# Performance work log

Hardware: AMD Instinct MI355X
Metric: run time of the kernel (lower is better)

Reference implementation:

```python
import jax, jax.numpy as jnp
import numpy as np

L, H, Wn, C = 2048, 768, 1024, 64


def setup_inputs() -> dict:
    key = jax.random.key(0)
    ks = jax.random.split(key, 12)
    s = 1.0 / np.sqrt(H)
    s3 = 1.0 / np.sqrt(3 * H)
    return {
        "tok_embs": jax.random.normal(ks[0], (L, H), jnp.float32),
        "wmask": jax.random.randint(ks[1], (L,), 0, Wn + 1),  # 1-indexed word positions, 0 = ignore
        "text_length": Wn,
        "label_embs": jax.random.normal(ks[2], (C, H), jnp.float32),
        "W_tok": jax.random.normal(ks[3], (H, 2 * H), jnp.float32) * s,
        "b_tok": jnp.zeros((2 * H,), jnp.float32),
        "W_lab": jax.random.normal(ks[4], (H, 2 * H), jnp.float32) * s,
        "b_lab": jnp.zeros((2 * H,), jnp.float32),
        "W1": jax.random.normal(ks[5], (3 * H, H), jnp.float32) * s3,
        "b1": jnp.zeros((H,), jnp.float32),
        "W2": jax.random.normal(ks[6], (H, 3), jnp.float32) * s,
        "b2": jnp.zeros((3,), jnp.float32),
    }


def reference(tok_embs, wmask, text_length, label_embs, W_tok, b_tok, W_lab, b_lab, W1, b1, W2, b2):
    Wd = text_length
    Hd = tok_embs.shape[-1]
    # --- word-level scatter pooling: we[wmask-1] = tok_embs where wmask > 0 ---
    # route masked-out tokens to a dummy row Wd, then drop it (jit-safe, no nonzero)
    tgt = jnp.where(wmask > 0, wmask - 1, Wd)
    we = jnp.zeros((Wd + 1, Hd), tok_embs.dtype).at[tgt].set(tok_embs)[:Wd]  # (W, H)
    # --- scorer ---
    t = (we @ W_tok + b_tok).reshape(Wd, 2, Hd)        # (W, 2, H)
    lb = (label_embs @ W_lab + b_lab).reshape(-1, 2, Hd)  # (C, 2, H)
    Cd = lb.shape[0]
    t0 = jnp.broadcast_to(t[:, None, 0, :], (Wd, Cd, Hd))
    l0 = jnp.broadcast_to(lb[None, :, 0, :], (Wd, Cd, Hd))
    prod = t[:, None, 1, :] * lb[None, :, 1, :]        # (W, C, H)
    cat = jnp.concatenate([t0, l0, prod], axis=-1)     # (W, C, 3H)
    h = jax.nn.relu(cat @ W1 + b1)                     # (W, C, H)
    scores = h @ W2 + b2                               # (W, C, 3)
    return scores
```

## Files before the change

### kernel.cpp

```cpp
#include <hip/hip_runtime.h>
#include <hip/hip_bf16.h>

static constexpr int Hd = 768;
static constexpr int H2 = 1536;
static constexpr int Cn = 64;

typedef __attribute__((ext_vector_type(8))) short short8;
typedef __attribute__((ext_vector_type(8))) _Float16 half8;
typedef __attribute__((ext_vector_type(4))) float f32x4;
typedef unsigned short us;

__device__ inline unsigned int f2bf2(float a, float b) {
    __hip_bfloat162 h = __float22bfloat162_rn(float2{a, b});
    return *reinterpret_cast<unsigned int*>(&h);
}

__device__ inline void split1(float x, us& h, us& l) {
    __hip_bfloat16 hb = __float2bfloat16(x);
    float hf = __bfloat162float(hb);
    __hip_bfloat16 lb_ = __float2bfloat16(x - hf);
    h = *reinterpret_cast<us*>(&hb);
    l = *reinterpret_cast<us*>(&lb_);
}

__device__ inline us f2b(float x) {
    __hip_bfloat16 b = __float2bfloat16(x);
    return *reinterpret_cast<us*>(&b);
}

__device__ inline us f2h(float x) {
    _Float16 h = (_Float16)x;
    return *reinterpret_cast<us*>(&h);
}

__device__ inline float b2f(us u) {
    __hip_bfloat16 b = *reinterpret_cast<__hip_bfloat16*>(&u);
    return __bfloat162float(b);
}

__device__ inline short8 hmul8(short8 a, short8 b) {
    half8 x = __builtin_bit_cast(half8, a);
    half8 y = __builtin_bit_cast(half8, b);
    half8 r = x * y;
    return __builtin_bit_cast(short8, r);
}

__device__ inline void gload16(const void* g, void* l) {
    __builtin_amdgcn_global_load_lds(
        (const __attribute__((address_space(1))) unsigned int*)g,
        (__attribute__((address_space(3))) unsigned int*)l, 16, 0, 0);
}

__global__ void k_init(int* widx, int Wd) {
    int i = blockIdx.x * 256 + threadIdx.x;
    if (i < Wd) widx[i] = -1;
}

__global__ void k_scatter(const int* __restrict__ wmask, int* widx, int L, int Wd) {
    int i = blockIdx.x * 256 + threadIdx.x;
    if (i < L) {
        int m = wmask[i];
        if (m > 0 && m <= Wd) atomicMax(&widx[m - 1], i);
    }
}

__global__ void k_build_we_split(const float4* __restrict__ tok, const int* __restrict__ widx,
                                 us* __restrict__ weh, us* __restrict__ wel, int Wd) {
    int i = blockIdx.x * 256 + threadIdx.x;
    if (i >= Wd * 192) return;
    int w = i / 192, c4 = i - w * 192;
    int idx = widx[w];
    float4 v = (idx >= 0) ? tok[idx * 192 + c4] : float4{0.f, 0.f, 0.f, 0.f};
    us hh[4], ll[4];
    split1(v.x, hh[0], ll[0]);
    split1(v.y, hh[1], ll[1]);
    split1(v.z, hh[2], ll[2]);
    split1(v.w, hh[3], ll[3]);
    size_t o = (size_t)w * Hd + c4 * 4;
    *(ushort4*)&weh[o] = ushort4{hh[0], hh[1], hh[2], hh[3]};
    *(ushort4*)&wel[o] = ushort4{ll[0], ll[1], ll[2], ll[3]};
}

struct TSArgs {
    const float* src[5];
    us* th[5];
    us* tl[5];
    int ld[5];
    int N[5];
    int fmt[5];
};
__global__ __launch_bounds__(256)
void k_tsplit(TSArgs a) {
    __shared__ float tile[64][65];
    const int z = blockIdx.z;
    const int n0 = blockIdx.x * 64, k0 = blockIdx.y * 64;
    if (n0 >= a.N[z]) return;
    const float* W = a.src[z];
    const int ld = a.ld[z];
    for (int idx = threadIdx.x; idx < 4096; idx += 256) {
        int kk = idx >> 6, nn = idx & 63;
        tile[kk][nn] = W[(size_t)(k0 + kk) * ld + n0 + nn];
    }
    __syncthreads();
    us* Th = a.th[z];
    us* Tl = a.tl[z];
    const int fmt = a.fmt[z];
    for (int idx = threadIdx.x; idx < 4096; idx += 256) {
        int nn = idx >> 6, kk = idx & 63;
        size_t o = (size_t)(n0 + nn) * Hd + k0 + kk;
        if (fmt) {
            Th[o] = f2h(tile[kk][nn]);
        } else {
            us h, l;
            split1(tile[kk][nn], h, l);
            Th[o] = h;
            Tl[o] = l;
        }
    }
}

__global__ __launch_bounds__(256)
void k_split(const float* __restrict__ x, int lda, int cols,
             us* __restrict__ h, us* __restrict__ l, int n4) {
    int i = blockIdx.x * 256 + threadIdx.x;
    if (i >= n4) return;
    int c4 = cols >> 2;
    int row = i / c4, cc = (i - row * c4) * 4;
    float4 v = *(const float4*)&x[(size_t)row * lda + cc];
    us hh[4], ll[4];
    split1(v.x, hh[0], ll[0]);
    split1(v.y, hh[1], ll[1]);
    split1(v.z, hh[2], ll[2]);
    split1(v.w, hh[3], ll[3]);
    size_t o = (size_t)row * cols + cc;
    *(ushort4*)&h[o] = ushort4{hh[0], hh[1], hh[2], hh[3]};
    *(ushort4*)&l[o] = ushort4{ll[0], ll[1], ll[2], ll[3]};
}

__global__ __launch_bounds__(256)
void k_gemm2(const us* __restrict__ Ah, const us* __restrict__ Al,
             const us* __restrict__ BhT, const us* __restrict__ BlT,
             float* __restrict__ Cpart, int M, int N, int K) {
    __shared__ __align__(16) us S[2][4][64 * 32];
    const int tid = threadIdx.x, wave = tid >> 6, lane = tid & 63;
    const int quad = lane >> 4, l15 = lane & 15;
    const int wm = wave & 1, wn = wave >> 1;
    const int m0 = blockIdx.y * 64, n0 = blockIdx.x * 64;
    const int Ks = K / gridDim.z, kbeg = blockIdx.z * Ks, kend = kbeg + Ks;
    float* C = Cpart + (size_t)blockIdx.z * M * N;

    const int srow = wave * 16 + (lane >> 2), soff = (lane & 3) * 8;
    const size_t gaB = (size_t)(m0 + srow) * K + soff;
    const size_t gbB = (size_t)(n0 + srow) * K + soff;
    const int lo = wave * 16 * 32;

    f32x4 acc[2][2];
#pragma unroll
    for (int a = 0; a < 2; ++a)
#pragma unroll
        for (int b = 0; b < 2; ++b) acc[a][b] = (f32x4){0.f, 0.f, 0.f, 0.f};

    auto stage = [&](int p, int k0) {
        gload16(Ah + gaB + k0, &S[p][0][lo]);
        gload16(Al + gaB + k0, &S[p][1][lo]);
        gload16(BhT + gbB + k0, &S[p][2][lo]);
        gload16(BlT + gbB + k0, &S[p][3][lo]);
    };

    int p = 0;
    stage(0, kbeg);
    for (int k0 = kbeg; k0 < kend; k0 += 32) {
        __syncthreads();
        if (k0 + 32 < kend) stage(p ^ 1, k0 + 32);
        short8 ah[2], al[2], bh[2], bl[2];
#pragma unroll
        for (int mt = 0; mt < 2; ++mt) {
            int off = (wm * 32 + mt * 16 + l15) * 32 + quad * 8;
            ah[mt] = *(const short8*)&S[p][0][off];
            al[mt] = *(const short8*)&S[p][1][off];
        }
#pragma unroll
        for (int nt = 0; nt < 2; ++nt) {
            int off = (wn * 32 + nt * 16 + l15) * 32 + quad * 8;
            bh[nt] = *(const short8*)&S[p][2][off];
            bl[nt] = *(const short8*)&S[p][3][off];
        }
#pragma unroll
        for (int mt = 0; mt < 2; ++mt)
#pragma unroll
            for (int nt = 0; nt < 2; ++nt) {
                acc[mt][nt] = __builtin_amdgcn_mfma_f32_16x16x32_bf16(al[mt], bh[nt], acc[mt][nt], 0, 0, 0);
                acc[mt][nt] = __builtin_amdgcn_mfma_f32_16x16x32_bf16(ah[mt], bl[nt], acc[mt][nt], 0, 0, 0);
                acc[mt][nt] = __builtin_amdgcn_mfma_f32_16x16x32_bf16(ah[mt], bh[nt], acc[mt][nt], 0, 0, 0);
            }
        p ^= 1;
    }
#pragma unroll
    for (int mt = 0; mt < 2; ++mt)
#pragma unroll
        for (int nt = 0; nt < 2; ++nt) {
            int col = n0 + wn * 32 + nt * 16 + l15;
#pragma unroll
            for (int reg = 0; reg < 4; ++reg) {
                int row = m0 + wm * 32 + mt * 16 + quad * 4 + reg;
                C[(size_t)row * N + col] = acc[mt][nt][reg];
            }
        }
}

__global__ __launch_bounds__(256)
void k_gemm3(const us* __restrict__ Ah, const us* __restrict__ Al,
             const us* __restrict__ BhT, const us* __restrict__ BlT,
             const float* __restrict__ bias, float* __restrict__ outF,
             us* __restrict__ sh, us* __restrict__ sl, us* __restrict__ bh16,
             int fp16out, int scols, int N, int K) {
    __shared__ __align__(16) us S[2][4][64 * 32];
    const int tid = threadIdx.x, wave = tid >> 6, lane = tid & 63;
    const int quad = lane >> 4, l15 = lane & 15;
    const int wm = wave & 1, wn = wave >> 1;
    const int m0 = blockIdx.y * 64, n0 = blockIdx.x * 64;

    const int srow = wave * 16 + (lane >> 2), soff = (lane & 3) * 8;
    const size_t gaB = (size_t)(m0 + srow) * K + soff;
    const size_t gbB = (size_t)(n0 + srow) * K + soff;
    const int lo = wave * 16 * 32;

    f32x4 acc[2][2];
#pragma unroll
    for (int a = 0; a < 2; ++a)
#pragma unroll
        for (int b = 0; b < 2; ++b) acc[a][b] = (f32x4){0.f, 0.f, 0.f, 0.f};

    auto stage = [&](int p, int k0) {
        gload16(Ah + gaB + k0, &S[p][0][lo]);
        gload16(Al + gaB + k0, &S[p][1][lo]);
        gload16(BhT + gbB + k0, &S[p][2][lo]);
        gload16(BlT + gbB + k0, &S[p][3][lo]);
    };

    int p = 0;
    stage(0, 0);
    for (int k0 = 0; k0 < K; k0 += 32) {
        __syncthreads();
        if (k0 + 32 < K) stage(p ^ 1, k0 + 32);
        short8 ah[2], al[2], bh[2], bl[2];
#pragma unroll
        for (int mt = 0; mt < 2; ++mt) {
            int off = (wm * 32 + mt * 16 + l15) * 32 + quad * 8;
            ah[mt] = *(const short8*)&S[p][0][off];
            al[mt] = *(const short8*)&S[p][1][off];
        }
#pragma unroll
        for (int nt = 0; nt < 2; ++nt) {
            int off = (wn * 32 + nt * 16 + l15) * 32 + quad * 8;
            bh[nt] = *(const short8*)&S[p][2][off];
            bl[nt] = *(const short8*)&S[p][3][off];
        }
#pragma unroll
        for (int mt = 0; mt < 2; ++mt)
#pragma unroll
            for (int nt = 0; nt < 2; ++nt) {
                acc[mt][nt] = __builtin_amdgcn_mfma_f32_16x16x32_bf16(al[mt], bh[nt], acc[mt][nt], 0, 0, 0);
                acc[mt][nt] = __builtin_amdgcn_mfma_f32_16x16x32_bf16(ah[mt], bl[nt], acc[mt][nt], 0, 0, 0);
                acc[mt][nt] = __builtin_amdgcn_mfma_f32_16x16x32_bf16(ah[mt], bh[nt], acc[mt][nt], 0, 0, 0);
            }
        p ^= 1;
    }
#pragma unroll
    for (int mt = 0; mt < 2; ++mt)
#pragma unroll
        for (int nt = 0; nt < 2; ++nt) {
            int col = n0 + wn * 32 + nt * 16 + l15;
            float bb = bias ? bias[col] : 0.f;
#pragma unroll
            for (int reg = 0; reg < 4; ++reg) {
                int row = m0 + wm * 32 + mt * 16 + quad * 4 + reg;
                float v = acc[mt][nt][reg] + bb;
                if (outF) outF[(size_t)row * N + col] = v;
                if (sh) {
                    if (col < scols) {
                        us h, l;
                        split1(v, h, l);
                        size_t o = (size_t)row * scols + col;
                        sh[o] = h;
                        sl[o] = l;
                    } else if (bh16) {
                        bh16[(size_t)row * scols + (col - scols)] = fp16out ? f2h(v) : f2b(v);
                    }
                }
            }
        }
}

__global__ __launch_bounds__(256)
void k_reduce(const float* __restrict__ part, int S, int MN, int N,
              const float* __restrict__ bias, float* __restrict__ outF,
              us* __restrict__ sh, us* __restrict__ sl, int scols,
              us* __restrict__ bh16, int fp16out) {
    int i = blockIdx.x * 256 + threadIdx.x;
    if (i >= MN) return;
    float v = 0.f;
    for (int s = 0; s < S; ++s) v += part[(size_t)s * MN + i];
    int row = i / N, col = i - row * N;
    if (bias) v += bias[col];
    if (outF) outF[i] = v;
    if (col < scols) {
        if (sh) {
            us h, l;
            split1(v, h, l);
            size_t o = (size_t)row * scols + col;
            sh[o] = h;
            sl[o] = l;
        }
    } else if (bh16) {
        bh16[(size_t)row * scols + (col - scols)] = fp16out ? f2h(v) : f2b(v);
    }
}

__global__ __launch_bounds__(256, 2)
void k_mfma10(const us* __restrict__ t1b,
              const us* __restrict__ W1ct,
              const us* __restrict__ lb1b,
              const float* __restrict__ Aw,
              const float* __restrict__ Bc,
              const float* __restrict__ W2,
              float* __restrict__ scr) {
    __shared__ __align__(16) us As[3][4096];
    __shared__ __align__(16) us Bs[3][4096];
    __shared__ __align__(16) us lbs[2][Hd];
    __shared__ float sred[2 * 128 * 3];

    const int tid = threadIdx.x, wave = tid >> 6, lane = tid & 63;
    const int quad = lane >> 4, l15 = lane & 15;
    const int wm = wave & 1, wn = wave >> 1;

    const int b = blockIdx.x;
    const int xcd = b & 7, slot = b >> 3;
    const int jx = slot >> 5;
    const int cp = slot & 31;
    const int c0 = cp * 2;
    const int jt = jx * 128, m0 = xcd * 128;

    for (int i = tid; i < 2 * 128 * 3; i += 256) sred[i] = 0.f;
    if (tid < 192) {
        int cc = tid / 96, o = (tid - cc * 96) * 8;
        *(short8*)&lbs[cc][o] = *(const short8*)&lb1b[(size_t)(c0 + cc) * Hd + o];
    }

    const int srow = (wave & 1) * 64 + lane;
    const int skq = (wave >> 1) * 8;
    const us* gA = W1ct + (size_t)(jt + srow) * Hd + skq;
    const us* gB = t1b + (size_t)(m0 + srow) * Hd + skq;

    f32x4 acc0[4][4], acc1[4][4];
#pragma unroll
    for (int mt = 0; mt < 4; ++mt)
#pragma unroll
        for (int nt = 0; nt < 4; ++nt) {
            acc0[mt][nt] = (f32x4){0.f, 0.f, 0.f, 0.f};
            acc1[mt][nt] = (f32x4){0.f, 0.f, 0.f, 0.f};
        }

    auto stageT = [&](int p, int k0) {
        gload16(gA + k0,      &As[p][wave * 512]);
        gload16(gA + k0 + 16, &As[p][(wave + 4) * 512]);
        gload16(gB + k0,      &Bs[p][wave * 512]);
        gload16(gB + k0 + 16, &Bs[p][(wave + 4) * 512]);
    };

    const int rbA = quad * 1024 + (wm * 64 + l15) * 8;
    const int rbB = quad * 1024 + (wn * 64 + l15) * 8;

    auto readFrags = [&](short8 (&af)[4], short8 (&bf)[4], short8& l0, short8& l1,
                         int buf, int k0) {
        const us* Ab = &As[buf][0];
        const us* Bb = &Bs[buf][0];
#pragma unroll
        for (int mt = 0; mt < 4; ++mt) af[mt] = *(const short8*)&Ab[rbA + mt * 128];
#pragma unroll
        for (int nt = 0; nt < 4; ++nt) bf[nt] = *(const short8*)&Bb[rbB + nt * 128];
        l0 = *(const short8*)&lbs[0][k0 + quad * 8];
        l1 = *(const short8*)&lbs[1][k0 + quad * 8];
    };

    auto cluster = [&](const short8 (&af)[4], const short8 (&bf)[4],
                       const short8& l0, const short8& l1) {
        __builtin_amdgcn_s_setprio(1);
#pragma unroll
        for (int mt = 0; mt < 4; ++mt) {
            short8 a0 = hmul8(af[mt], l0);
            short8 a1 = hmul8(af[mt], l1);
#pragma unroll
            for (int nt = 0; nt < 4; ++nt) {
                acc0[mt][nt] = __builtin_amdgcn_mfma_f32_16x16x32_f16(
                    __builtin_bit_cast(half8, a0),
                    __builtin_bit_cast(half8, bf[nt]), acc0[mt][nt], 0, 0, 0);
                acc1[mt][nt] = __builtin_amdgcn_mfma_f32_16x16x32_f16(
                    __builtin_bit_cast(half8, a1),
                    __builtin_bit_cast(half8, bf[nt]), acc1[mt][nt], 0, 0, 0);
            }
        }
        __builtin_amdgcn_s_setprio(0);
    };

    __syncthreads();

    stageT(0, 0);
    stageT(1, 32);
    asm volatile("s_waitcnt vmcnt(4)" ::: "memory");
    __builtin_amdgcn_s_barrier();
    __builtin_amdgcn_sched_barrier(0);

    short8 afA[4], bfA[4], lvA0, lvA1;
    short8 afB[4], bfB[4], lvB0, lvB1;
    readFrags(afA, bfA, lvA0, lvA1, 0, 0);

    int bc = 0, bn = 1, bs = 2;
    for (int i = 0; i < 24; i += 2) {
        if (i + 1 < 24) {
            asm volatile("s_waitcnt vmcnt(0)" ::: "memory");
            __builtin_amdgcn_s_barrier();
            __builtin_amdgcn_sched_barrier(0);
            readFrags(afB, bfB, lvB0, lvB1, bn, (i + 1) * 32);
            if (i + 2 < 24) stageT(bs, (i + 2) * 32);
            int t = bc; bc = bn; bn = bs; bs = t;
            __builtin_amdgcn_sched_barrier(0);
        }
        cluster(afA, bfA, lvA0, lvA1);
        if (i + 2 < 24) {
            asm volatile("s_waitcnt vmcnt(0)" ::: "memory");
            __builtin_amdgcn_s_barrier();
            __builtin_amdgcn_sched_barrier(0);
            readFrags(afA, bfA, lvA0, lvA1, bn, (i + 2) * 32);
            if (i + 3 < 24) stageT(bs, (i + 3) * 32);
            int t = bc; bc = bn; bn = bs; bs = t;
            __builtin_amdgcn_sched_barrier(0);
        }
        cluster(afB, bfB, lvB0, lvB1);
    }

    float bcv0[4][4], bcv1[4][4], w2v[4][4][3];
#pragma unroll
    for (int mt = 0; mt < 4; ++mt) {
        const int jb = jt + wm * 64 + mt * 16 + quad * 4;
        float4 b4 = *(const float4*)&Bc[(size_t)c0 * Hd + jb];
        bcv0[mt][0] = b4.x; bcv0[mt][1] = b4.y; bcv0[mt][2] = b4.z; bcv0[mt][3] = b4.w;
        float4 b5 = *(const float4*)&Bc[(size_t)(c0 + 1) * Hd + jb];
        bcv1[mt][0] = b5.x; bcv1[mt][1] = b5.y; bcv1[mt][2] = b5.z; bcv1[mt][3] = b5.w;
#pragma unroll
        for (int reg = 0; reg < 4; ++reg)
#pragma unroll
            for (int r = 0; r < 3; ++r) w2v[mt][reg][r] = W2[(jb + reg) * 3 + r];
    }

    auto reduce_c = [&](const f32x4 (&ac)[4][4], const float (&bcv)[4][4], int cc) {
#pragma unroll
        for (int nt = 0; nt < 4; ++nt) {
            const int w = m0 + wn * 64 + nt * 16 + l15;
            const float* awp = Aw + (size_t)w * Hd + jt + wm * 64;
            float s0 = 0.f, s1 = 0.f, s2 = 0.f;
#pragma unroll
            for (int mt = 0; mt < 4; ++mt) {
                float4 a4 = *(const float4*)&awp[mt * 16 + quad * 4];
                float av[4] = {a4.x, a4.y, a4.z, a4.w};
#pragma unroll
                for (int reg = 0; reg < 4; ++reg) {
                    float h = ac[mt][nt][reg] + av[reg] + bcv[mt][reg];
                    h = h > 0.f ? h : 0.f;
                    s0 += h * w2v[mt][reg][0];
                    s1 += h * w2v[mt][reg][1];
                    s2 += h * w2v[mt][reg][2];
                }
            }
            s0 += __shfl_xor(s0, 16); s0 += __shfl_xor(s0, 32);
            s1 += __shfl_xor(s1, 16); s1 += __shfl_xor(s1, 32);
            s2 += __shfl_xor(s2, 16); s2 += __shfl_xor(s2, 32);
            if (quad == 0) {
                const int wl = wn * 64 + nt * 16 + l15;
                atomicAdd(&sred[cc * 384 + wl * 3 + 0], s0);
                atomicAdd(&sred[cc * 384 + wl * 3 + 1], s1);
                atomicAdd(&sred[cc * 384 + wl * 3 + 2], s2);
            }
        }
    };
    reduce_c(acc0, bcv0, 0);
    reduce_c(acc1, bcv1, 1);
    __syncthreads();

    float* slab = scr + ((size_t)jx * 1024 * Cn + (size_t)m0 * Cn) * 3;
    for (int i = tid; i < 2 * 128 * 3; i += 256) {
        int cc = i / 384, j = i - cc * 384;
        int wl = j / 3, r = j - wl * 3;
        slab[((size_t)wl * Cn + (c0 + cc)) * 3 + r] = sred[i];
    }
}

__global__ __launch_bounds__(256)
void k_scores(const float* __restrict__ scr, const float* __restrict__ b2,
              float* __restrict__ out, int n) {
    int i = blockIdx.x * 256 + threadIdx.x;
    if (i >= n) return;
    float v = b2[i % 3];
#pragma unroll
    for (int s = 0; s < 6; ++s) v += scr[(size_t)s * n + i];
    out[i] = v;
}

extern "C" void kernel_launch(void* const* d_in, const int* in_sizes, int n_in,
                              void* d_out, int out_size, void* d_ws, size_t ws_size,
                              hipStream_t stream) {
    const float* tok    = (const float*)d_in[0];
    const int*   wmask  = (const int*)d_in[1];
    const float* labe   = (const float*)d_in[3];
    const float* W_tok  = (const float*)d_in[4];
    const float* b_tok  = (const float*)d_in[5];
    const float* W_lab  = (const float*)d_in[6];
    const float* b_lab  = (const float*)d_in[7];
    const float* W1     = (const float*)d_in[8];
    const float* b1     = (const float*)d_in[9];
    const float* W2     = (const float*)d_in[10];
    const float* b2     = (const float*)d_in[11];
    float* out = (float*)d_out;

    const int L  = in_sizes[1];
    const int Wd = out_size / (Cn * 3);

    char* ws = (char*)d_ws;
    size_t off = 0;
    auto alloc = [&](size_t bytes) { char* p = ws + off; off += (bytes + 255) & ~(size_t)255; return p; };
    int*   widx  = (int*)alloc(4096);
    float* Abuf  = (float*)alloc((size_t)Wd * Hd * 4);
    float* Bbuf  = (float*)alloc((size_t)Cn * Hd * 4);
    us* W1ct  = (us*)alloc((size_t)Hd * Hd * 2);
    us* W1cl  = (us*)alloc((size_t)Hd * Hd * 2);
    us* t1b   = (us*)alloc((size_t)Wd * Hd * 2);
    us* lb1b  = (us*)alloc((size_t)Cn * Hd * 2);
    float* scr = (float*)alloc((size_t)6 * Wd * Cn * 3 * 4);
    us* WtTh  = (us*)alloc((size_t)H2 * Hd * 2);
    us* WtTl  = (us*)alloc((size_t)H2 * Hd * 2);
    us* WlTh  = (us*)alloc((size_t)H2 * Hd * 2);
    us* WlTl  = (us*)alloc((size_t)H2 * Hd * 2);
    us* W1aTh = (us*)alloc((size_t)Hd * Hd * 2);
    us* W1aTl = (us*)alloc((size_t)Hd * Hd * 2);
    us* W1bTh = (us*)alloc((size_t)Hd * Hd * 2);
    us* W1bTl = (us*)alloc((size_t)Hd * Hd * 2);
    us* weh   = (us*)alloc((size_t)Wd * Hd * 2);
    us* wel   = (us*)alloc((size_t)Wd * Hd * 2);
    us* lah   = (us*)alloc((size_t)Cn * Hd * 2);
    us* lal   = (us*)alloc((size_t)Cn * Hd * 2);
    us* t0h   = (us*)alloc((size_t)Wd * Hd * 2);
    us* t0l   = (us*)alloc((size_t)Wd * Hd * 2);
    us* lb0h  = (us*)alloc((size_t)Cn * Hd * 2);
    us* lb0l  = (us*)alloc((size_t)Cn * Hd * 2);
    float* part = (float*)alloc((size_t)8 * Cn * H2 * 4);

    k_init<<<(Wd + 255) / 256, 256, 0, stream>>>(widx, Wd);
    k_scatter<<<(L + 255) / 256, 256, 0, stream>>>(wmask, widx, L, Wd);
    k_build_we_split<<<(Wd * 192 + 255) / 256, 256, 0, stream>>>((const float4*)tok, widx, weh, wel, Wd);

    TSArgs ts;
    ts.src[0] = W_tok;  ts.th[0] = WtTh;  ts.tl[0] = WtTl;  ts.ld[0] = H2; ts.N[0] = H2; ts.fmt[0] = 0;
    ts.src[1] = W_lab;  ts.th[1] = WlTh;  ts.tl[1] = WlTl;  ts.ld[1] = H2; ts.N[1] = H2; ts.fmt[1] = 0;
    ts.src[2] = W1;                         ts.th[2] = W1aTh; ts.tl[2] = W1aTl; ts.ld[2] = Hd; ts.N[2] = Hd; ts.fmt[2] = 0;
    ts.src[3] = W1 + (size_t)Hd * Hd;       ts.th[3] = W1bTh; ts.tl[3] = W1bTl; ts.ld[3] = Hd; ts.N[3] = Hd; ts.fmt[3] = 0;
    ts.src[4] = W1 + (size_t)2 * Hd * Hd;   ts.th[4] = W1ct;  ts.tl[4] = W1cl;  ts.ld[4] = Hd; ts.N[4] = Hd; ts.fmt[4] = 1;
    k_tsplit<<<dim3(H2 / 64, Hd / 64, 5), 256, 0, stream>>>(ts);

    k_split<<<(Cn * Hd / 4 + 255) / 256, 256, 0, stream>>>(labe, Hd, Hd, lah, lal, Cn * Hd / 4);

    k_gemm3<<<dim3(H2 / 64, Wd / 64), 256, 0, stream>>>(weh, wel, WtTh, WtTl, b_tok,
                                                        nullptr, t0h, t0l, t1b, 1, Hd, H2, Hd);

    k_gemm2<<<dim3(H2 / 64, 1, 8), 256, 0, stream>>>(lah, lal, WlTh, WlTl, part, Cn, H2, Hd);
    k_reduce<<<(Cn * H2 + 255) / 256, 256, 0, stream>>>(part, 8, Cn * H2, H2, b_lab, nullptr, lb0h, lb0l, Hd, lb1b, 1);

    k_gemm3<<<dim3(Hd / 64, Wd / 64), 256, 0, stream>>>(t0h, t0l, W1aTh, W1aTl, nullptr,
                                                        Abuf, nullptr, nullptr, nullptr, 0, 0, Hd, Hd);

    k_gemm2<<<dim3(Hd / 64, 1, 8), 256, 0, stream>>>(lb0h, lb0l, W1bTh, W1bTl, part, Cn, Hd, Hd);
    k_reduce<<<(Cn * Hd + 255) / 256, 256, 0, stream>>>(part, 8, Cn * Hd, Hd, b1, Bbuf, nullptr, nullptr, Hd, nullptr, 0);

    k_mfma10<<<1536, 256, 0, stream>>>(t1b, W1ct, lb1b, Abuf, Bbuf, W2, scr);

    k_scores<<<(Wd * Cn * 3 + 255) / 256, 256, 0, stream>>>(scr, b2, out, Wd * Cn * 3);
}
```

Before: 250.4 us.

## Halve word tile in fused MLP kernel to raise occupancy and block count

The main fused kernel now uses a 128(j) x 64(word) tile per block instead of 128x128. Each wave owns 32 j-columns across all 64 words, so accumulators drop from 32 to 16 vectors. The grid doubles to 3072 blocks and launch bounds allow 3 blocks per CU. The goal is fewer registers, less LDS and better latency hiding. The cost is lower MFMA data reuse per loaded fragment, more global traffic for the W1c tile and label vectors, and a B stage that now issues one load per wave.

```diff
diff --git a/kernel.cpp b/kernel.cpp
--- a/kernel.cpp
+++ b/kernel.cpp
@@ -317,8 +317,8 @@
     }
 }
 
-__global__ __launch_bounds__(256, 2)
-void k_mfma10(const us* __restrict__ t1b,
+__global__ __launch_bounds__(256, 3)
+void k_mfma11(const us* __restrict__ t1b,
               const us* __restrict__ W1ct,
               const us* __restrict__ lb1b,
               const float* __restrict__ Aw,
@@ -326,78 +326,79 @@
               const float* __restrict__ W2,
               float* __restrict__ scr) {
     __shared__ __align__(16) us As[3][4096];
-    __shared__ __align__(16) us Bs[3][4096];
+    __shared__ __align__(16) us Bs[3][2048];
     __shared__ __align__(16) us lbs[2][Hd];
-    __shared__ float sred[2 * 128 * 3];
+    __shared__ float sred[2 * 64 * 3];
 
     const int tid = threadIdx.x, wave = tid >> 6, lane = tid & 63;
     const int quad = lane >> 4, l15 = lane & 15;
-    const int wm = wave & 1, wn = wave >> 1;
+    const int wj = wave;
 
     const int b = blockIdx.x;
     const int xcd = b & 7, slot = b >> 3;
-    const int jx = slot >> 5;
-    const int cp = slot & 31;
+    const int jx = slot >> 6;
+    const int rem = slot & 63;
+    const int mm = rem >> 5;
+    const int cp = rem & 31;
     const int c0 = cp * 2;
-    const int jt = jx * 128, m0 = xcd * 128;
-
-    for (int i = tid; i < 2 * 128 * 3; i += 256) sred[i] = 0.f;
+    const int jt = jx * 128, m0 = (xcd * 2 + mm) * 64;
+
+    for (int i = tid; i < 2 * 64 * 3; i += 256) sred[i] = 0.f;
     if (tid < 192) {
         int cc = tid / 96, o = (tid - cc * 96) * 8;
         *(short8*)&lbs[cc][o] = *(const short8*)&lb1b[(size_t)(c0 + cc) * Hd + o];
     }
 
-    const int srow = (wave & 1) * 64 + lane;
-    const int skq = (wave >> 1) * 8;
-    const us* gA = W1ct + (size_t)(jt + srow) * Hd + skq;
-    const us* gB = t1b + (size_t)(m0 + srow) * Hd + skq;
-
-    f32x4 acc0[4][4], acc1[4][4];
-#pragma unroll
-    for (int mt = 0; mt < 4; ++mt)
+    const int srowA = (wave & 1) * 64 + lane;
+    const int skqA = (wave >> 1) * 8;
+    const us* gA = W1ct + (size_t)(jt + srowA) * Hd + skqA;
+    const us* gB = t1b + (size_t)(m0 + lane) * Hd + wave * 8;
+
+    f32x4 acc0[2][4], acc1[2][4];
+#pragma unroll
+    for (int jf = 0; jf < 2; ++jf)
 #pragma unroll
         for (int nt = 0; nt < 4; ++nt) {
-            acc0[mt][nt] = (f32x4){0.f, 0.f, 0.f, 0.f};
-            acc1[mt][nt] = (f32x4){0.f, 0.f, 0.f, 0.f};
+            acc0[jf][nt] = (f32x4){0.f, 0.f, 0.f, 0.f};
+            acc1[jf][nt] = (f32x4){0.f, 0.f, 0.f, 0.f};
         }
 
     auto stageT = [&](int p, int k0) {
         gload16(gA + k0,      &As[p][wave * 512]);
         gload16(gA + k0 + 16, &As[p][(wave + 4) * 512]);
         gload16(gB + k0,      &Bs[p][wave * 512]);
-        gload16(gB + k0 + 16, &Bs[p][(wave + 4) * 512]);
     };
 
-    const int rbA = quad * 1024 + (wm * 64 + l15) * 8;
-    const int rbB = quad * 1024 + (wn * 64 + l15) * 8;
-
-    auto readFrags = [&](short8 (&af)[4], short8 (&bf)[4], short8& l0, short8& l1,
+    const int rbA = quad * 1024 + (wj * 32 + l15) * 8;
+    const int rbB = quad * 512 + l15 * 8;
+
+    auto readFrags = [&](short8 (&af)[2], short8 (&bf)[4], short8& l0, short8& l1,
                          int buf, int k0) {
         const us* Ab = &As[buf][0];
         const us* Bb = &Bs[buf][0];
 #pragma unroll
-        for (int mt = 0; mt < 4; ++mt) af[mt] = *(const short8*)&Ab[rbA + mt * 128];
+        for (int jf = 0; jf < 2; ++jf) af[jf] = *(const short8*)&Ab[rbA + jf * 128];
 #pragma unroll
         for (int nt = 0; nt < 4; ++nt) bf[nt] = *(const short8*)&Bb[rbB + nt * 128];
         l0 = *(const short8*)&lbs[0][k0 + quad * 8];
         l1 = *(const short8*)&lbs[1][k0 + quad * 8];
     };
 
-    auto cluster = [&](const short8 (&af)[4], const short8 (&bf)[4],
+    auto cluster = [&](const short8 (&af)[2], const short8 (&bf)[4],
                        const short8& l0, const short8& l1) {
         __builtin_amdgcn_s_setprio(1);
 #pragma unroll
-        for (int mt = 0; mt < 4; ++mt) {
-            short8 a0 = hmul8(af[mt], l0);
-            short8 a1 = hmul8(af[mt], l1);
+        for (int jf = 0; jf < 2; ++jf) {
+            short8 a0 = hmul8(af[jf], l0);
+            short8 a1 = hmul8(af[jf], l1);
 #pragma unroll
             for (int nt = 0; nt < 4; ++nt) {
-                acc0[mt][nt] = __builtin_amdgcn_mfma_f32_16x16x32_f16(
+                acc0[jf][nt] = __builtin_amdgcn_mfma_f32_16x16x32_f16(
                     __builtin_bit_cast(half8, a0),
-                    __builtin_bit_cast(half8, bf[nt]), acc0[mt][nt], 0, 0, 0);
-                acc1[mt][nt] = __builtin_amdgcn_mfma_f32_16x16x32_f16(
+                    __builtin_bit_cast(half8, bf[nt]), acc0[jf][nt], 0, 0, 0);
+                acc1[jf][nt] = __builtin_amdgcn_mfma_f32_16x16x32_f16(
                     __builtin_bit_cast(half8, a1),
-                    __builtin_bit_cast(half8, bf[nt]), acc1[mt][nt], 0, 0, 0);
+                    __builtin_bit_cast(half8, bf[nt]), acc1[jf][nt], 0, 0, 0);
             }
         }
         __builtin_amdgcn_s_setprio(0);
@@ -407,12 +408,12 @@
 
     stageT(0, 0);
     stageT(1, 32);
-    asm volatile("s_waitcnt vmcnt(4)" ::: "memory");
+    asm volatile("s_waitcnt vmcnt(3)" ::: "memory");
     __builtin_amdgcn_s_barrier();
     __builtin_amdgcn_sched_barrier(0);
 
-    short8 afA[4], bfA[4], lvA0, lvA1;
-    short8 afB[4], bfB[4], lvB0, lvB1;
+    short8 afA[2], bfA[4], lvA0, lvA1;
+    short8 afB[2], bfB[4], lvB0, lvB1;
     readFrags(afA, bfA, lvA0, lvA1, 0, 0);
 
     int bc = 0, bn = 1, bs = 2;
@@ -439,57 +440,65 @@
         cluster(afB, bfB, lvB0, lvB1);
     }
 
-    float bcv0[4][4], bcv1[4][4], w2v[4][4][3];
-#pragma unroll
-    for (int mt = 0; mt < 4; ++mt) {
-        const int jb = jt + wm * 64 + mt * 16 + quad * 4;
+    float bcv0[2][4], bcv1[2][4], w2v[2][4][3];
+#pragma unroll
+    for (int jf = 0; jf < 2; ++jf) {
+        const int jb = jt + wj * 32 + jf * 16 + quad * 4;
         float4 b4 = *(const float4*)&Bc[(size_t)c0 * Hd + jb];
-        bcv0[mt][0] = b4.x; bcv0[mt][1] = b4.y; bcv0[mt][2] = b4.z; bcv0[mt][3] = b4.w;
+        bcv0[jf][0] = b4.x; bcv0[jf][1] = b4.y; bcv0[jf][2] = b4.z; bcv0[jf][3] = b4.w;
         float4 b5 = *(const float4*)&Bc[(size_t)(c0 + 1) * Hd + jb];
-        bcv1[mt][0] = b5.x; bcv1[mt][1] = b5.y; bcv1[mt][2] = b5.z; bcv1[mt][3] = b5.w;
+        bcv1[jf][0] = b5.x; bcv1[jf][1] = b5.y; bcv1[jf][2] = b5.z; bcv1[jf][3] = b5.w;
 #pragma unroll
         for (int reg = 0; reg < 4; ++reg)
 #pragma unroll
-            for (int r = 0; r < 3; ++r) w2v[mt][reg][r] = W2[(jb + reg) * 3 + r];
-    }
-
-    auto reduce_c = [&](const f32x4 (&ac)[4][4], const float (&bcv)[4][4], int cc) {
-#pragma unroll
-        for (int nt = 0; nt < 4; ++nt) {
-            const int w = m0 + wn * 64 + nt * 16 + l15;
-            const float* awp = Aw + (size_t)w * Hd + jt + wm * 64;
-            float s0 = 0.f, s1 = 0.f, s2 = 0.f;
-#pragma unroll
-            for (int mt = 0; mt < 4; ++mt) {
-                float4 a4 = *(const float4*)&awp[mt * 16 + quad * 4];
-                float av[4] = {a4.x, a4.y, a4.z, a4.w};
-#pragma unroll
-                for (int reg = 0; reg < 4; ++reg) {
-                    float h = ac[mt][nt][reg] + av[reg] + bcv[mt][reg];
-                    h = h > 0.f ? h : 0.f;
-                    s0 += h * w2v[mt][reg][0];
-                    s1 += h * w2v[mt][reg][1];
-                    s2 += h * w2v[mt][reg][2];
-                }
+            for (int r = 0; r < 3; ++r) w2v[jf][reg][r] = W2[(jb + reg) * 3 + r];
+    }
+
+#pragma unroll
+    for (int nt = 0; nt < 4; ++nt) {
+        const int w = m0 + nt * 16 + l15;
+        const float* awp = Aw + (size_t)w * Hd + jt + wj * 32;
+        float s00 = 0.f, s01 = 0.f, s02 = 0.f;
+        float s10 = 0.f, s11 = 0.f, s12 = 0.f;
+#pragma unroll
+        for (int jf = 0; jf < 2; ++jf) {
+            float4 a4 = *(const float4*)&awp[jf * 16 + quad * 4];
+            float av[4] = {a4.x, a4.y, a4.z, a4.w};
+#pragma unroll
+            for (int reg = 0; reg < 4; ++reg) {
+                float h0 = acc0[jf][nt][reg] + av[reg] + bcv0[jf][reg];
+                h0 = h0 > 0.f ? h0 : 0.f;
+                s00 += h0 * w2v[jf][reg][0];
+                s01 += h0 * w2v[jf][reg][1];
+                s02 += h0 * w2v[jf][reg][2];
+                float h1 = acc1[jf][nt][reg] + av[reg] + bcv1[jf][reg];
+                h1 = h1 > 0.f ? h1 : 0.f;
+                s10 += h1 * w2v[jf][reg][0];
+                s11 += h1 * w2v[jf][reg][1];
+                s12 += h1 * w2v[jf][reg][2];
             }
-            s0 += __shfl_xor(s0, 16); s0 += __shfl_xor(s0, 32);
-            s1 += __shfl_xor(s1, 16); s1 += __shfl_xor(s1, 32);
-            s2 += __shfl_xor(s2, 16); s2 += __shfl_xor(s2, 32);
-            if (quad == 0) {
-                const int wl = wn * 64 + nt * 16 + l15;
-                atomicAdd(&sred[cc * 384 + wl * 3 + 0], s0);
-                atomicAdd(&sred[cc * 384 + wl * 3 + 1], s1);
-                atomicAdd(&sred[cc * 384 + wl * 3 + 2], s2);
-            }
-        }
-    };
-    reduce_c(acc0, bcv0, 0);
-    reduce_c(acc1, bcv1, 1);
+        }
+        s00 += __shfl_xor(s00, 16); s00 += __shfl_xor(s00, 32);
+        s01 += __shfl_xor(s01, 16); s01 += __shfl_xor(s01, 32);
+        s02 += __shfl_xor(s02, 16); s02 += __shfl_xor(s02, 32);
+        s10 += __shfl_xor(s10, 16); s10 += __shfl_xor(s10, 32);
+        s11 += __shfl_xor(s11, 16); s11 += __shfl_xor(s11, 32);
+        s12 += __shfl_xor(s12, 16); s12 += __shfl_xor(s12, 32);
+        if (quad == 0) {
+            const int wl = nt * 16 + l15;
+            atomicAdd(&sred[wl * 3 + 0], s00);
+            atomicAdd(&sred[wl * 3 + 1], s01);
+            atomicAdd(&sred[wl * 3 + 2], s02);
+            atomicAdd(&sred[192 + wl * 3 + 0], s10);
+            atomicAdd(&sred[192 + wl * 3 + 1], s11);
+            atomicAdd(&sred[192 + wl * 3 + 2], s12);
+        }
+    }
     __syncthreads();
 
     float* slab = scr + ((size_t)jx * 1024 * Cn + (size_t)m0 * Cn) * 3;
-    for (int i = tid; i < 2 * 128 * 3; i += 256) {
-        int cc = i / 384, j = i - cc * 384;
+    for (int i = tid; i < 2 * 64 * 3; i += 256) {
+        int cc = i / 192, j = i - cc * 192;
         int wl = j / 3, r = j - wl * 3;
         slab[((size_t)wl * Cn + (c0 + cc)) * 3 + r] = sred[i];
     }
@@ -580,7 +589,7 @@
     k_gemm2<<<dim3(Hd / 64, 1, 8), 256, 0, stream>>>(lb0h, lb0l, W1bTh, W1bTl, part, Cn, Hd, Hd);
     k_reduce<<<(Cn * Hd + 255) / 256, 256, 0, stream>>>(part, 8, Cn * Hd, Hd, b1, Bbuf, nullptr, nullptr, Hd, nullptr, 0);
 
-    k_mfma10<<<1536, 256, 0, stream>>>(t1b, W1ct, lb1b, Abuf, Bbuf, W2, scr);
+    k_mfma11<<<3072, 256, 0, stream>>>(t1b, W1ct, lb1b, Abuf, Bbuf, W2, scr);
 
     k_scores<<<(Wd * Cn * 3 + 255) / 256, 256, 0, stream>>>(scr, b2, out, Wd * Cn * 3);
 }
```

After: 275.7 us. +10.1%, slower.

## Give each wave private LDS staging to remove block barriers in main GEMM loop

Applied to the files above, without the earlier changes.

Each wave now loads its own A and B tile rows into a private double-buffered LDS region, so the per-k-step workgroup barriers are replaced by per-wave vmcnt/lgkmcnt waits. This removes barrier stalls between waves. In exchange, A and B rows shared across waves are fetched redundantly, doubling global/L2 load traffic, and LDS use rises.

```diff
diff --git a/kernel.cpp b/kernel.cpp
--- a/kernel.cpp
+++ b/kernel.cpp
@@ -318,15 +318,15 @@
 }
 
 __global__ __launch_bounds__(256, 2)
-void k_mfma10(const us* __restrict__ t1b,
+void k_mfma12(const us* __restrict__ t1b,
               const us* __restrict__ W1ct,
               const us* __restrict__ lb1b,
               const float* __restrict__ Aw,
               const float* __restrict__ Bc,
               const float* __restrict__ W2,
               float* __restrict__ scr) {
-    __shared__ __align__(16) us As[3][4096];
-    __shared__ __align__(16) us Bs[3][4096];
+    __shared__ __align__(16) us As[4][2][2048];
+    __shared__ __align__(16) us Bs[4][2][2048];
     __shared__ __align__(16) us lbs[2][Hd];
     __shared__ float sred[2 * 128 * 3];
 
@@ -347,10 +347,8 @@
         *(short8*)&lbs[cc][o] = *(const short8*)&lb1b[(size_t)(c0 + cc) * Hd + o];
     }
 
-    const int srow = (wave & 1) * 64 + lane;
-    const int skq = (wave >> 1) * 8;
-    const us* gA = W1ct + (size_t)(jt + srow) * Hd + skq;
-    const us* gB = t1b + (size_t)(m0 + srow) * Hd + skq;
+    const us* gA = W1ct + (size_t)(jt + wm * 64 + lane) * Hd;
+    const us* gB = t1b + (size_t)(m0 + wn * 64 + lane) * Hd;
 
     f32x4 acc0[4][4], acc1[4][4];
 #pragma unroll
@@ -361,24 +359,24 @@
             acc1[mt][nt] = (f32x4){0.f, 0.f, 0.f, 0.f};
         }
 
-    auto stageT = [&](int p, int k0) {
-        gload16(gA + k0,      &As[p][wave * 512]);
-        gload16(gA + k0 + 16, &As[p][(wave + 4) * 512]);
-        gload16(gB + k0,      &Bs[p][wave * 512]);
-        gload16(gB + k0 + 16, &Bs[p][(wave + 4) * 512]);
+    auto stage = [&](int p, int k0) {
+#pragma unroll
+        for (int q = 0; q < 4; ++q) {
+            gload16(gA + k0 + q * 8, &As[wave][p][q * 512]);
+            gload16(gB + k0 + q * 8, &Bs[wave][p][q * 512]);
+        }
     };
 
-    const int rbA = quad * 1024 + (wm * 64 + l15) * 8;
-    const int rbB = quad * 1024 + (wn * 64 + l15) * 8;
+    const int rb = quad * 512 + l15 * 8;
 
     auto readFrags = [&](short8 (&af)[4], short8 (&bf)[4], short8& l0, short8& l1,
                          int buf, int k0) {
-        const us* Ab = &As[buf][0];
-        const us* Bb = &Bs[buf][0];
-#pragma unroll
-        for (int mt = 0; mt < 4; ++mt) af[mt] = *(const short8*)&Ab[rbA + mt * 128];
-#pragma unroll
-        for (int nt = 0; nt < 4; ++nt) bf[nt] = *(const short8*)&Bb[rbB + nt * 128];
+        const us* Ab = &As[wave][buf][0];
+        const us* Bb = &Bs[wave][buf][0];
+#pragma unroll
+        for (int mt = 0; mt < 4; ++mt) af[mt] = *(const short8*)&Ab[rb + mt * 128];
+#pragma unroll
+        for (int nt = 0; nt < 4; ++nt) bf[nt] = *(const short8*)&Bb[rb + nt * 128];
         l0 = *(const short8*)&lbs[0][k0 + quad * 8];
         l1 = *(const short8*)&lbs[1][k0 + quad * 8];
     };
@@ -405,38 +403,32 @@
 
     __syncthreads();
 
-    stageT(0, 0);
-    stageT(1, 32);
-    asm volatile("s_waitcnt vmcnt(4)" ::: "memory");
-    __builtin_amdgcn_s_barrier();
-    __builtin_amdgcn_sched_barrier(0);
-
-    short8 afA[4], bfA[4], lvA0, lvA1;
-    short8 afB[4], bfB[4], lvB0, lvB1;
-    readFrags(afA, bfA, lvA0, lvA1, 0, 0);
-
-    int bc = 0, bn = 1, bs = 2;
+    stage(0, 0);
+    stage(1, 32);
+    asm volatile("s_waitcnt vmcnt(8)" ::: "memory");
+    short8 afC[4], bfC[4], lvC0, lvC1;
+    short8 afN[4], bfN[4], lvN0, lvN1;
+    readFrags(afC, bfC, lvC0, lvC1, 0, 0);
+
     for (int i = 0; i < 24; i += 2) {
         if (i + 1 < 24) {
             asm volatile("s_waitcnt vmcnt(0)" ::: "memory");
-            __builtin_amdgcn_s_barrier();
+            readFrags(afN, bfN, lvN0, lvN1, (i + 1) & 1, (i + 1) * 32);
             __builtin_amdgcn_sched_barrier(0);
-            readFrags(afB, bfB, lvB0, lvB1, bn, (i + 1) * 32);
-            if (i + 2 < 24) stageT(bs, (i + 2) * 32);
-            int t = bc; bc = bn; bn = bs; bs = t;
+            asm volatile("s_waitcnt lgkmcnt(10)" ::: "memory");
+            if (i + 2 < 24) stage(i & 1, (i + 2) * 32);
             __builtin_amdgcn_sched_barrier(0);
         }
-        cluster(afA, bfA, lvA0, lvA1);
+        cluster(afC, bfC, lvC0, lvC1);
         if (i + 2 < 24) {
             asm volatile("s_waitcnt vmcnt(0)" ::: "memory");
-            __builtin_amdgcn_s_barrier();
+            readFrags(afC, bfC, lvC0, lvC1, (i + 2) & 1, (i + 2) * 32);
             __builtin_amdgcn_sched_barrier(0);
-            readFrags(afA, bfA, lvA0, lvA1, bn, (i + 2) * 32);
-            if (i + 3 < 24) stageT(bs, (i + 3) * 32);
-            int t = bc; bc = bn; bn = bs; bs = t;
+            asm volatile("s_waitcnt lgkmcnt(10)" ::: "memory");
+            if (i + 3 < 24) stage((i + 1) & 1, (i + 3) * 32);
             __builtin_amdgcn_sched_barrier(0);
         }
-        cluster(afB, bfB, lvB0, lvB1);
+        cluster(afN, bfN, lvN0, lvN1);
     }
 
     float bcv0[4][4], bcv1[4][4], w2v[4][4][3];
@@ -580,7 +572,7 @@
     k_gemm2<<<dim3(Hd / 64, 1, 8), 256, 0, stream>>>(lb0h, lb0l, W1bTh, W1bTl, part, Cn, Hd, Hd);
     k_reduce<<<(Cn * Hd + 255) / 256, 256, 0, stream>>>(part, 8, Cn * Hd, Hd, b1, Bbuf, nullptr, nullptr, Hd, nullptr, 0);
 
-    k_mfma10<<<1536, 256, 0, stream>>>(t1b, W1ct, lb1b, Abuf, Bbuf, W2, scr);
+    k_mfma12<<<1536, 256, 0, stream>>>(t1b, W1ct, lb1b, Abuf, Bbuf, W2, scr);
 
     k_scores<<<(Wd * Cn * 3 + 255) / 256, 256, 0, stream>>>(scr, b2, out, Wd * Cn * 3);
 }
```

Result: slower. 380.0 us (+51.8%).
